# Performance work log

Hardware: AMD Instinct MI355X
Metric: run time of the kernel (lower is better)

The kernel has to match this reference:

```python
import jax, jax.numpy as jnp
import numpy as np

N = 100000   # nodes
E = 800000   # edges (avg degree 8)
D = 384      # feature dim (fixed by GraphConv(384,384))
OUT = 2      # out_channels


def setup_inputs() -> dict:
    key = jax.random.key(0)
    ks = jax.random.split(key, 10)
    s = 1.0 / np.sqrt(D)
    x = jax.random.normal(ks[0], (N, D), jnp.float32)
    edge_index = jax.random.randint(ks[1], (2, E), 0, N, dtype=jnp.int64)
    edge_weight = jax.random.uniform(ks[2], (E,), jnp.float32)
    return {
        "x": x,
        "edge_index": edge_index,
        "edge_weight": edge_weight,
        "W_rel1": jax.random.normal(ks[3], (D, D), jnp.float32) * s,
        "b_rel1": jnp.zeros((D,), jnp.float32),
        "W_root1": jax.random.normal(ks[4], (D, D), jnp.float32) * s,
        "W_rel2": jax.random.normal(ks[5], (D, D), jnp.float32) * s,
        "b_rel2": jnp.zeros((D,), jnp.float32),
        "W_root2": jax.random.normal(ks[6], (D, D), jnp.float32) * s,
        "W_lin": jax.random.normal(ks[7], (D, OUT), jnp.float32) * s,
        "b_lin": jnp.zeros((OUT,), jnp.float32),
    }


def _graph_conv(x, src, dst, ew, W_rel, b_rel, W_root):
    # PyG GraphConv (aggr='mean'): lin_rel(mean_j(ew_j * x_src_j)) + lin_root(x)
    msgs = ew[:, None] * x[src]                                   # [E, D] gather
    agg = jax.ops.segment_sum(msgs, dst, num_segments=N)          # [N, D] scatter
    cnt = jax.ops.segment_sum(jnp.ones_like(ew), dst, num_segments=N)
    mean = agg / jnp.maximum(cnt, 1.0)[:, None]
    return mean @ W_rel + b_rel + x @ W_root


def reference(x, edge_index, edge_weight,
              W_rel1, b_rel1, W_root1,
              W_rel2, b_rel2, W_root2,
              W_lin, b_lin):
    src, dst = edge_index[0], edge_index[1]
    h = jax.nn.relu(_graph_conv(x, src, dst, edge_weight, W_rel1, b_rel1, W_root1))
    # dropout(p=0.3) is identity in eval mode
    y = jax.nn.relu(_graph_conv(h, src, dst, edge_weight, W_rel2, b_rel2, W_root2))
    out = jax.nn.sigmoid(y @ W_lin + b_lin)                        # [N, OUT]
    return (out, y)
```

## Files before the change

### kernel.cpp

```cpp
#include <hip/hip_runtime.h>
#include <hip/hip_bf16.h>

typedef __bf16 bf16_t;
typedef bf16_t bf16x8 __attribute__((ext_vector_type(8)));
typedef float f32x4 __attribute__((ext_vector_type(4)));

typedef __attribute__((address_space(3))) unsigned int lds_u32;
typedef __attribute__((address_space(1))) unsigned int glb_u32;

__device__ __forceinline__ float bflo(unsigned int p){ union{unsigned int u; float f;} c; c.u = p << 16; return c.f; }
__device__ __forceinline__ float bfhi(unsigned int p){ union{unsigned int u; float f;} c; c.u = p & 0xffff0000u; return c.f; }
__device__ __forceinline__ unsigned int f2bfu(float f){
  union{float f; unsigned int u;} c; c.f = f;
  return (c.u + 0x7fffu + ((c.u >> 16) & 1u)) >> 16;
}

__global__ void k_cast_x(const float4* __restrict__ x, uint2* __restrict__ xb, int nq){
  int stride = gridDim.x * blockDim.x;
  for (int i = blockIdx.x * blockDim.x + threadIdx.x; i < nq; i += stride){
    float4 v = x[i];
    uint2 o;
    o.x = f2bfu(v.x) | (f2bfu(v.y) << 16);
    o.y = f2bfu(v.z) | (f2bfu(v.w) << 16);
    xb[i] = o;
  }
}

__global__ void k_castT_w4(const float* __restrict__ W0, const float* __restrict__ W1,
                           const float* __restrict__ W2, const float* __restrict__ W3,
                           unsigned short* __restrict__ T0, unsigned short* __restrict__ T1,
                           unsigned short* __restrict__ T2, unsigned short* __restrict__ T3){
  const float* W; unsigned short* T;
  switch (blockIdx.y){
    case 0: W = W0; T = T0; break;
    case 1: W = W1; T = T1; break;
    case 2: W = W2; T = T2; break;
    default: W = W3; T = T3; break;
  }
  int idx = blockIdx.x * 256 + threadIdx.x;
  int k = idx / 384, n = idx - k * 384;
  T[n * 384 + k] = (unsigned short)f2bfu(W[idx]);
}

__global__ void k_deg(const int* __restrict__ dst, int* __restrict__ deg, int E){
  int stride = gridDim.x * blockDim.x;
  for (int e = blockIdx.x * blockDim.x + threadIdx.x; e < E; e += stride)
    atomicAdd(&deg[dst[e]], 1);
}

__global__ void k_scan1(const int* __restrict__ deg, int* __restrict__ incl,
                        int* __restrict__ bsum, int n){
  __shared__ int wsum[16];
  int t = threadIdx.x, l = t & 63, w = t >> 6;
  int i = blockIdx.x * 1024 + t;
  int v = (i < n) ? deg[i] : 0;
  int xv = v;
  #pragma unroll
  for (int s = 1; s < 64; s <<= 1){
    int y = __shfl_up(xv, s, 64);
    if (l >= s) xv += y;
  }
  if (l == 63) wsum[w] = xv;
  __syncthreads();
  int off = 0;
  for (int k2 = 0; k2 < w; ++k2) off += wsum[k2];
  if (i < n) incl[i] = off + xv;
  if (t == 0){
    int tot = 0;
    for (int k2 = 0; k2 < 16; ++k2) tot += wsum[k2];
    bsum[blockIdx.x] = tot;
  }
}

__global__ void k_scan2(int* __restrict__ bsum, int nb){
  __shared__ int wtot;
  int t = threadIdx.x, l = t & 63, w = t >> 6;
  int v = (t < nb) ? bsum[t] : 0;
  int xv = v;
  #pragma unroll
  for (int s = 1; s < 64; s <<= 1){
    int y = __shfl_up(xv, s, 64);
    if (l >= s) xv += y;
  }
  if (t == 63) wtot = xv;
  __syncthreads();
  int off = (w == 1) ? wtot : 0;
  if (t < nb) bsum[t] = off + xv - v;
}

__global__ void k_scan3(const int* __restrict__ incl, const int* __restrict__ bsum,
                        const int* __restrict__ deg, int* __restrict__ rowptr,
                        int* __restrict__ cursor, int n){
  int i = blockIdx.x * 256 + threadIdx.x;
  if (i < n){
    int r = incl[i] + bsum[i >> 10];
    rowptr[i + 1] = r;
    cursor[i] = r - deg[i];
  }
  if (i == 0) rowptr[0] = 0;
}

__global__ void k_fill(const int* __restrict__ src, const int* __restrict__ dst, const float* __restrict__ ew,
                       int* __restrict__ cursor, int2* __restrict__ csr, int E){
  int stride = gridDim.x * blockDim.x;
  for (int e = blockIdx.x * blockDim.x + threadIdx.x; e < E; e += stride){
    int d = dst[e];
    int pos = atomicAdd(&cursor[d], 1);
    int2 c; c.x = src[e]; c.y = __float_as_int(ew[e]);
    csr[pos] = c;
  }
}

__global__ void k_agg(const unsigned short* __restrict__ X, unsigned short* __restrict__ OUT,
                      const int* __restrict__ rowptr, const int2* __restrict__ csr, int n_nodes){
  int w = threadIdx.x >> 6, l = threadIdx.x & 63;
  int node = blockIdx.x * 4 + w;
  if (node >= n_nodes) return;
  int e0 = rowptr[node], e1 = rowptr[node + 1];
  float a0=0,a1=0,a2=0,a3=0,a4=0,a5=0;
  const unsigned int* X32 = (const unsigned int*)X;
  int e = e0;
  for (; e + 2 <= e1; e += 2){
    int2 c0 = csr[e], c1 = csr[e + 1];
    const unsigned int* x0 = X32 + (long)c0.x * 192;
    const unsigned int* x1 = X32 + (long)c1.x * 192;
    unsigned int p0 = x0[l], p1 = x0[l + 64], p2 = x0[l + 128];
    unsigned int q0 = x1[l], q1 = x1[l + 64], q2 = x1[l + 128];
    float w0 = __int_as_float(c0.y), w1 = __int_as_float(c1.y);
    a0 += w0 * bflo(p0); a1 += w0 * bfhi(p0);
    a2 += w0 * bflo(p1); a3 += w0 * bfhi(p1);
    a4 += w0 * bflo(p2); a5 += w0 * bfhi(p2);
    a0 += w1 * bflo(q0); a1 += w1 * bfhi(q0);
    a2 += w1 * bflo(q1); a3 += w1 * bfhi(q1);
    a4 += w1 * bflo(q2); a5 += w1 * bfhi(q2);
  }
  if (e < e1){
    int2 c0 = csr[e];
    const unsigned int* x0 = X32 + (long)c0.x * 192;
    unsigned int p0 = x0[l], p1 = x0[l + 64], p2 = x0[l + 128];
    float w0 = __int_as_float(c0.y);
    a0 += w0 * bflo(p0); a1 += w0 * bfhi(p0);
    a2 += w0 * bflo(p1); a3 += w0 * bfhi(p1);
    a4 += w0 * bflo(p2); a5 += w0 * bfhi(p2);
  }
  int degn = e1 - e0;
  float inv = 1.0f / (float)(degn > 1 ? degn : 1);
  unsigned int* O32 = (unsigned int*)OUT + (long)node * 192;
  O32[l]       = f2bfu(a0 * inv) | (f2bfu(a1 * inv) << 16);
  O32[l + 64]  = f2bfu(a2 * inv) | (f2bfu(a3 * inv) << 16);
  O32[l + 128] = f2bfu(a4 * inv) | (f2bfu(a5 * inv) << 16);
}

template<int OUT_BF16>
__global__ __launch_bounds__(256) void k_gemm(
    const unsigned short* __restrict__ A1, const unsigned short* __restrict__ B1,
    const unsigned short* __restrict__ A2, const unsigned short* __restrict__ B2,
    const float* __restrict__ bias, void* __restrict__ Cout, int NN, int q, int r)
{
  __shared__ __align__(16) unsigned short lsA[2 * 128 * 32];
  __shared__ __align__(16) unsigned short lsB[2 * 128 * 32];
  int t = threadIdx.x;
  int w = t >> 6, l = t & 63;

  int lin = blockIdx.y * 3 + blockIdx.x;
  int xcd = lin & 7, idx = lin >> 3;
  int nl = idx + ((xcd < r) ? xcd * (q + 1) : r * (q + 1) + (xcd - r) * q);
  int mt = nl / 3, nt = nl - mt * 3;
  int m0 = mt * 128;
  int n0 = nt * 128;
  int wrow = (w & 1) * 64, wcol = (w >> 1) * 64;

  f32x4 acc[4][4] = {};

  int ar = t >> 2, ac = t & 3;
  int sw = (ar >> 1) & 3;
  int acs = (ac ^ sw) * 8;
  int ra0 = m0 + ar;       if (ra0 >= NN) ra0 = NN - 1;
  int ra1 = m0 + 64 + ar;  if (ra1 >= NN) ra1 = NN - 1;
  int rb0 = n0 + ar, rb1 = n0 + 64 + ar;

  char* lsAb = (char*)lsA;
  char* lsBb = (char*)lsB;

#define STAGE(buf, kk) do { \
    const unsigned short* Ag = ((kk) < 12) ? A1 : A2; \
    const unsigned short* Bg = ((kk) < 12) ? B1 : B2; \
    int kc = ((((kk) < 12) ? (kk) : (kk) - 12) << 5) + acs; \
    __builtin_amdgcn_global_load_lds((glb_u32*)(Ag + (long)ra0 * 384 + kc), (lds_u32*)(lsAb + (buf) * 8192 + w * 1024), 16, 0, 0); \
    __builtin_amdgcn_global_load_lds((glb_u32*)(Ag + (long)ra1 * 384 + kc), (lds_u32*)(lsAb + (buf) * 8192 + 4096 + w * 1024), 16, 0, 0); \
    __builtin_amdgcn_global_load_lds((glb_u32*)(Bg + (long)rb0 * 384 + kc), (lds_u32*)(lsBb + (buf) * 8192 + w * 1024), 16, 0, 0); \
    __builtin_amdgcn_global_load_lds((glb_u32*)(Bg + (long)rb1 * 384 + kc), (lds_u32*)(lsBb + (buf) * 8192 + 4096 + w * 1024), 16, 0, 0); \
  } while (0)

  STAGE(0, 0);
  __syncthreads();

  int rA = wrow + (l & 15);
  int rB = wcol + (l & 15);
  int swA = (rA >> 1) & 3, swB = (rB >> 1) & 3;
  int kchunk = l >> 4;
  int offA = ((kchunk ^ swA) * 8);
  int offB = ((kchunk ^ swB) * 8);

  for (int kk = 0; kk < 24; ++kk){
    int cur = kk & 1;
    if (kk < 23) STAGE(cur ^ 1, kk + 1);
    const unsigned short* bA = lsA + cur * 4096;
    const unsigned short* bB = lsB + cur * 4096;
    bf16x8 af[4], bfr[4];
    #pragma unroll
    for (int mi = 0; mi < 4; ++mi) af[mi]  = *(const bf16x8*)&bA[(rA + mi * 16) * 32 + offA];
    #pragma unroll
    for (int ni = 0; ni < 4; ++ni) bfr[ni] = *(const bf16x8*)&bB[(rB + ni * 16) * 32 + offB];
    #pragma unroll
    for (int mi = 0; mi < 4; ++mi)
      #pragma unroll
      for (int ni = 0; ni < 4; ++ni)
        acc[mi][ni] = __builtin_amdgcn_mfma_f32_16x16x32_bf16(af[mi], bfr[ni], acc[mi][ni], 0, 0, 0);
    __syncthreads();
  }
#undef STAGE

  int colb = l & 15, rowb = (l >> 4) * 4;
  #pragma unroll
  for (int mi = 0; mi < 4; ++mi){
    #pragma unroll
    for (int ni = 0; ni < 4; ++ni){
      f32x4 v = acc[mi][ni];
      int col = n0 + wcol + ni * 16 + colb;
      float bcol = bias[col];
      #pragma unroll
      for (int rr = 0; rr < 4; ++rr){
        int row = m0 + wrow + mi * 16 + rowb + rr;
        if (row < NN){
          float val = fmaxf(v[rr] + bcol, 0.0f);
          if (OUT_BF16) ((unsigned short*)Cout)[(long)row * 384 + col] = (unsigned short)f2bfu(val);
          else          ((float*)Cout)[(long)row * 384 + col] = val;
        }
      }
    }
  }
}

__global__ void k_out(const float* __restrict__ Y, const float* __restrict__ WL,
                      const float* __restrict__ bl, float* __restrict__ out, int n_nodes){
  int w = threadIdx.x >> 6, l = threadIdx.x & 63;
  int node = blockIdx.x * 4 + w;
  if (node >= n_nodes) return;
  const float* yr = Y + (long)node * 384;
  float s0 = 0.f, s1 = 0.f;
  #pragma unroll
  for (int j = 0; j < 6; ++j){
    int d = l + 64 * j;
    float v = yr[d];
    s0 += v * WL[2 * d];
    s1 += v * WL[2 * d + 1];
  }
  #pragma unroll
  for (int m = 32; m; m >>= 1){
    s0 += __shfl_xor(s0, m);
    s1 += __shfl_xor(s1, m);
  }
  if (l == 0){
    out[(long)node * 2]     = 1.f / (1.f + expf(-(s0 + bl[0])));
    out[(long)node * 2 + 1] = 1.f / (1.f + expf(-(s1 + bl[1])));
  }
}

extern "C" void kernel_launch(void* const* d_in, const int* in_sizes, int n_in,
                              void* d_out, int out_size, void* d_ws, size_t ws_size,
                              hipStream_t stream) {
  const float* x      = (const float*)d_in[0];
  const int*   ei     = (const int*)d_in[1];
  const float* ew     = (const float*)d_in[2];
  const float* Wrel1  = (const float*)d_in[3];
  const float* brel1  = (const float*)d_in[4];
  const float* Wroot1 = (const float*)d_in[5];
  const float* Wrel2  = (const float*)d_in[6];
  const float* brel2  = (const float*)d_in[7];
  const float* Wroot2 = (const float*)d_in[8];
  const float* Wlin   = (const float*)d_in[9];
  const float* blin   = (const float*)d_in[10];

  const int NN = in_sizes[0] / 384;
  const int E  = in_sizes[2];
  const int* src = ei;
  const int* dst = ei + E;

  char* p = (char*)d_ws;
  auto carve = [&](size_t bytes) -> void* {
    void* r = (void*)p;
    p += (bytes + 255) & ~(size_t)255;
    return r;
  };
  int*   deg     = (int*)carve((size_t)NN * 4);
  int*   rowptr  = (int*)carve((size_t)(NN + 1) * 4);
  int*   cursor  = (int*)carve((size_t)NN * 4);
  int*   incl    = (int*)carve((size_t)NN * 4);
  int*   bsum    = (int*)carve(1024);
  int2*  csr     = (int2*)carve((size_t)E * 8);
  unsigned short* xb  = (unsigned short*)carve((size_t)NN * 384 * 2);
  unsigned short* m1b = (unsigned short*)carve((size_t)NN * 384 * 2);
  unsigned short* hb  = (unsigned short*)carve((size_t)NN * 384 * 2);
  unsigned short* WT1 = (unsigned short*)carve(384 * 384 * 2);
  unsigned short* WT2 = (unsigned short*)carve(384 * 384 * 2);
  unsigned short* WT3 = (unsigned short*)carve(384 * 384 * 2);
  unsigned short* WT4 = (unsigned short*)carve(384 * 384 * 2);

  float* out = (float*)d_out;
  float* Y   = out + (size_t)NN * 2;

  int nScanB = (NN + 1023) / 1024;

  hipMemsetAsync(deg, 0, (size_t)NN * 4, stream);
  k_cast_x<<<2048, 256, 0, stream>>>((const float4*)x, (uint2*)xb, NN * 96);
  dim3 wg(576, 4);
  k_castT_w4<<<wg, 256, 0, stream>>>(Wrel1, Wroot1, Wrel2, Wroot2, WT1, WT2, WT3, WT4);
  k_deg<<<1024, 256, 0, stream>>>(dst, deg, E);
  k_scan1<<<nScanB, 1024, 0, stream>>>(deg, incl, bsum, NN);
  k_scan2<<<1, 128, 0, stream>>>(bsum, nScanB);
  k_scan3<<<(NN + 255) / 256, 256, 0, stream>>>(incl, bsum, deg, rowptr, cursor, NN);
  k_fill<<<1024, 256, 0, stream>>>(src, dst, ew, cursor, csr, E);

  int aggBlocks = (NN + 3) / 4;
  k_agg<<<aggBlocks, 256, 0, stream>>>(xb, m1b, rowptr, csr, NN);

  int gy = (NN + 127) / 128;
  int nwg = 3 * gy, q = nwg >> 3, r = nwg & 7;
  dim3 ggrid(3, gy);
  k_gemm<1><<<ggrid, 256, 0, stream>>>(m1b, WT1, xb, WT2, brel1, (void*)hb, NN, q, r);

  k_agg<<<aggBlocks, 256, 0, stream>>>(hb, m1b, rowptr, csr, NN);

  k_gemm<0><<<ggrid, 256, 0, stream>>>(m1b, WT3, hb, WT4, brel2, (void*)Y, NN, q, r);

  k_out<<<aggBlocks, 256, 0, stream>>>(Y, Wlin, blin, out, NN);
}
```

Baseline: 590.4 us.

## Restructure GEMM: direct B loads, K=64 steps, LDS-staged epilogue, fused output head

The GEMM now stages only the A tile in LDS with 64-wide K steps and an XOR swizzle. The B fragments are loaded straight from global memory into registers, and the K loop is fully unrolled with explicit waitcnt and barriers. The bf16 epilogue goes through LDS so stores are coalesced 16-byte writes. The second GEMM also computes the final linear projection, using shuffle reductions and atomicAdds into a logits buffer, and this replaces the separate k_out kernel that reread Y. In exchange it adds a memset and a small sigmoid kernel, plus atomic contention across the three column tiles.

```diff
diff --git a/kernel.cpp b/kernel.cpp
--- a/kernel.cpp
+++ b/kernel.cpp
@@ -155,116 +155,147 @@
 __global__ __launch_bounds__(256) void k_gemm(
     const unsigned short* __restrict__ A1, const unsigned short* __restrict__ B1,
     const unsigned short* __restrict__ A2, const unsigned short* __restrict__ B2,
-    const float* __restrict__ bias, void* __restrict__ Cout, int NN, int q, int r)
+    const float* __restrict__ bias, void* __restrict__ Cout,
+    const float* __restrict__ WL, float* __restrict__ olog,
+    int NN, int q, int r)
 {
-  __shared__ __align__(16) unsigned short lsA[2 * 128 * 32];
-  __shared__ __align__(16) unsigned short lsB[2 * 128 * 32];
+  __shared__ __align__(16) unsigned short lsA[2 * 128 * 64];
   int t = threadIdx.x;
   int w = t >> 6, l = t & 63;
 
-  int lin = blockIdx.y * 3 + blockIdx.x;
+  int lin = blockIdx.x;
   int xcd = lin & 7, idx = lin >> 3;
   int nl = idx + ((xcd < r) ? xcd * (q + 1) : r * (q + 1) + (xcd - r) * q);
   int mt = nl / 3, nt = nl - mt * 3;
-  int m0 = mt * 128;
-  int n0 = nt * 128;
+  int m0 = mt * 128, n0 = nt * 128;
   int wrow = (w & 1) * 64, wcol = (w >> 1) * 64;
 
   f32x4 acc[4][4] = {};
 
-  int ar = t >> 2, ac = t & 3;
-  int sw = (ar >> 1) & 3;
-  int acs = (ac ^ sw) * 8;
-  int ra0 = m0 + ar;       if (ra0 >= NN) ra0 = NN - 1;
-  int ra1 = m0 + 64 + ar;  if (ra1 >= NN) ra1 = NN - 1;
-  int rb0 = n0 + ar, rb1 = n0 + 64 + ar;
-
-  char* lsAb = (char*)lsA;
-  char* lsBb = (char*)lsB;
-
-#define STAGE(buf, kk) do { \
-    const unsigned short* Ag = ((kk) < 12) ? A1 : A2; \
-    const unsigned short* Bg = ((kk) < 12) ? B1 : B2; \
-    int kc = ((((kk) < 12) ? (kk) : (kk) - 12) << 5) + acs; \
-    __builtin_amdgcn_global_load_lds((glb_u32*)(Ag + (long)ra0 * 384 + kc), (lds_u32*)(lsAb + (buf) * 8192 + w * 1024), 16, 0, 0); \
-    __builtin_amdgcn_global_load_lds((glb_u32*)(Ag + (long)ra1 * 384 + kc), (lds_u32*)(lsAb + (buf) * 8192 + 4096 + w * 1024), 16, 0, 0); \
-    __builtin_amdgcn_global_load_lds((glb_u32*)(Bg + (long)rb0 * 384 + kc), (lds_u32*)(lsBb + (buf) * 8192 + w * 1024), 16, 0, 0); \
-    __builtin_amdgcn_global_load_lds((glb_u32*)(Bg + (long)rb1 * 384 + kc), (lds_u32*)(lsBb + (buf) * 8192 + 4096 + w * 1024), 16, 0, 0); \
+  int srow = t >> 3, sj = t & 7;
+  int sjx = sj ^ (srow & 7);
+
+  int rAb = wrow + (l & 15);
+  int jx  = (l & 15) & 7;
+  int kq  = l >> 4;
+  int rB  = n0 + wcol + (l & 15);
+  int koff = kq * 8;
+
+#define STAGE(buf, kk_) do { \
+    const unsigned short* Ag_ = ((kk_) < 6) ? A1 : A2; \
+    int kc_ = (((kk_) < 6) ? (kk_) : (kk_) - 6) << 6; \
+    _Pragma("unroll") \
+    for (int p_ = 0; p_ < 4; ++p_){ \
+      int ra_ = m0 + p_ * 32 + srow; if (ra_ >= NN) ra_ = NN - 1; \
+      __builtin_amdgcn_global_load_lds((glb_u32*)(Ag_ + (long)ra_ * 384 + kc_ + sjx * 8), \
+          (lds_u32*)((char*)lsA + (buf) * 16384 + p_ * 4096 + w * 1024), 16, 0, 0); \
+    } \
   } while (0)
 
   STAGE(0, 0);
-  __syncthreads();
-
-  int rA = wrow + (l & 15);
-  int rB = wcol + (l & 15);
-  int swA = (rA >> 1) & 3, swB = (rB >> 1) & 3;
-  int kchunk = l >> 4;
-  int offA = ((kchunk ^ swA) * 8);
-  int offB = ((kchunk ^ swB) * 8);
-
-  for (int kk = 0; kk < 24; ++kk){
+
+  #pragma unroll
+  for (int kk = 0; kk < 12; ++kk){
     int cur = kk & 1;
-    if (kk < 23) STAGE(cur ^ 1, kk + 1);
-    const unsigned short* bA = lsA + cur * 4096;
-    const unsigned short* bB = lsB + cur * 4096;
-    bf16x8 af[4], bfr[4];
-    #pragma unroll
-    for (int mi = 0; mi < 4; ++mi) af[mi]  = *(const bf16x8*)&bA[(rA + mi * 16) * 32 + offA];
-    #pragma unroll
-    for (int ni = 0; ni < 4; ++ni) bfr[ni] = *(const bf16x8*)&bB[(rB + ni * 16) * 32 + offB];
+    asm volatile("s_waitcnt vmcnt(0)" ::: "memory");
+    asm volatile("s_barrier" ::: "memory");
+    __builtin_amdgcn_sched_barrier(0);
+
+    const unsigned short* Bg = (kk < 6) ? B1 : B2;
+    int kc = ((kk < 6) ? kk : kk - 6) << 6;
+    bf16x8 bfr[2][4];
+    #pragma unroll
+    for (int s = 0; s < 2; ++s)
+      #pragma unroll
+      for (int ni = 0; ni < 4; ++ni)
+        bfr[s][ni] = *(const bf16x8*)&Bg[(long)(rB + ni * 16) * 384 + kc + s * 32 + koff];
+    __builtin_amdgcn_sched_barrier(0);
+
+    if (kk < 11) STAGE(cur ^ 1, kk + 1);
+    __builtin_amdgcn_sched_barrier(0);
+
+    const char* bA = (const char*)lsA + cur * 16384;
+    #pragma unroll
+    for (int s = 0; s < 2; ++s){
+      bf16x8 af[4];
+      #pragma unroll
+      for (int mi = 0; mi < 4; ++mi)
+        af[mi] = *(const bf16x8*)(bA + ((rAb + mi * 16) << 7) + ((((s << 2) + kq) ^ jx) << 4));
+      #pragma unroll
+      for (int mi = 0; mi < 4; ++mi)
+        #pragma unroll
+        for (int ni = 0; ni < 4; ++ni)
+          acc[mi][ni] = __builtin_amdgcn_mfma_f32_16x16x32_bf16(af[mi], bfr[s][ni], acc[mi][ni], 0, 0, 0);
+    }
+  }
+#undef STAGE
+
+  int colb = l & 15;
+  if (OUT_BF16){
+    __syncthreads();
+    unsigned short* lr = (unsigned short*)lsA;
     #pragma unroll
     for (int mi = 0; mi < 4; ++mi)
       #pragma unroll
-      for (int ni = 0; ni < 4; ++ni)
-        acc[mi][ni] = __builtin_amdgcn_mfma_f32_16x16x32_bf16(af[mi], bfr[ni], acc[mi][ni], 0, 0, 0);
-    __syncthreads();
-  }
-#undef STAGE
-
-  int colb = l & 15, rowb = (l >> 4) * 4;
-  #pragma unroll
-  for (int mi = 0; mi < 4; ++mi){
-    #pragma unroll
-    for (int ni = 0; ni < 4; ++ni){
-      f32x4 v = acc[mi][ni];
-      int col = n0 + wcol + ni * 16 + colb;
-      float bcol = bias[col];
-      #pragma unroll
-      for (int rr = 0; rr < 4; ++rr){
-        int row = m0 + wrow + mi * 16 + rowb + rr;
-        if (row < NN){
-          float val = fmaxf(v[rr] + bcol, 0.0f);
-          if (OUT_BF16) ((unsigned short*)Cout)[(long)row * 384 + col] = (unsigned short)f2bfu(val);
-          else          ((float*)Cout)[(long)row * 384 + col] = val;
+      for (int ni = 0; ni < 4; ++ni){
+        f32x4 v = acc[mi][ni];
+        int col = wcol + ni * 16 + colb;
+        float bcol = bias[n0 + col];
+        #pragma unroll
+        for (int rr = 0; rr < 4; ++rr){
+          int row = wrow + mi * 16 + kq * 4 + rr;
+          lr[row * 128 + col] = (unsigned short)f2bfu(fmaxf(v[rr] + bcol, 0.0f));
         }
       }
+    __syncthreads();
+    unsigned short* Cb = (unsigned short*)Cout;
+    #pragma unroll
+    for (int p = 0; p < 8; ++p){
+      int idx16 = p * 256 + t;
+      int row = idx16 >> 4, chunk = idx16 & 15;
+      int rg = m0 + row;
+      if (rg < NN)
+        *(uint4*)((char*)Cb + (long)rg * 768 + n0 * 2 + chunk * 16) =
+            *(const uint4*)((const char*)lsA + idx16 * 16);
     }
-  }
-}
-
-__global__ void k_out(const float* __restrict__ Y, const float* __restrict__ WL,
-                      const float* __restrict__ bl, float* __restrict__ out, int n_nodes){
-  int w = threadIdx.x >> 6, l = threadIdx.x & 63;
-  int node = blockIdx.x * 4 + w;
-  if (node >= n_nodes) return;
-  const float* yr = Y + (long)node * 384;
-  float s0 = 0.f, s1 = 0.f;
-  #pragma unroll
-  for (int j = 0; j < 6; ++j){
-    int d = l + 64 * j;
-    float v = yr[d];
-    s0 += v * WL[2 * d];
-    s1 += v * WL[2 * d + 1];
-  }
-  #pragma unroll
-  for (int m = 32; m; m >>= 1){
-    s0 += __shfl_xor(s0, m);
-    s1 += __shfl_xor(s1, m);
-  }
-  if (l == 0){
-    out[(long)node * 2]     = 1.f / (1.f + expf(-(s0 + bl[0])));
-    out[(long)node * 2 + 1] = 1.f / (1.f + expf(-(s1 + bl[1])));
-  }
+  } else {
+    float* Cf = (float*)Cout;
+    #pragma unroll
+    for (int mi = 0; mi < 4; ++mi){
+      float po[4][2] = {};
+      #pragma unroll
+      for (int ni = 0; ni < 4; ++ni){
+        f32x4 v = acc[mi][ni];
+        int col = n0 + wcol + ni * 16 + colb;
+        float bcol = bias[col];
+        float w0 = WL[col * 2], w1 = WL[col * 2 + 1];
+        #pragma unroll
+        for (int rr = 0; rr < 4; ++rr){
+          int row = m0 + wrow + mi * 16 + kq * 4 + rr;
+          float val = fmaxf(v[rr] + bcol, 0.0f);
+          if (row < NN) Cf[(long)row * 384 + col] = val;
+          po[rr][0] += val * w0;
+          po[rr][1] += val * w1;
+        }
+      }
+      #pragma unroll
+      for (int rr = 0; rr < 4; ++rr)
+        #pragma unroll
+        for (int o = 0; o < 2; ++o){
+          float v = po[rr][o];
+          v += __shfl_xor(v, 1); v += __shfl_xor(v, 2);
+          v += __shfl_xor(v, 4); v += __shfl_xor(v, 8);
+          int row = m0 + wrow + mi * 16 + kq * 4 + rr;
+          if (colb == 0 && row < NN) atomicAdd(&olog[row * 2 + o], v);
+        }
+    }
+  }
+}
+
+__global__ void k_sig(const float* __restrict__ olog, const float* __restrict__ bl,
+                      float* __restrict__ out, int n2){
+  int i = blockIdx.x * 256 + threadIdx.x;
+  if (i < n2) out[i] = 1.f / (1.f + expf(-(olog[i] + bl[i & 1])));
 }
 
 extern "C" void kernel_launch(void* const* d_in, const int* in_sizes, int n_in,
@@ -298,6 +329,7 @@
   int*   cursor  = (int*)carve((size_t)NN * 4);
   int*   incl    = (int*)carve((size_t)NN * 4);
   int*   bsum    = (int*)carve(1024);
+  float* olog    = (float*)carve((size_t)NN * 2 * 4);
   int2*  csr     = (int2*)carve((size_t)E * 8);
   unsigned short* xb  = (unsigned short*)carve((size_t)NN * 384 * 2);
   unsigned short* m1b = (unsigned short*)carve((size_t)NN * 384 * 2);
@@ -313,6 +345,7 @@
   int nScanB = (NN + 1023) / 1024;
 
   hipMemsetAsync(deg, 0, (size_t)NN * 4, stream);
+  hipMemsetAsync(olog, 0, (size_t)NN * 8, stream);
   k_cast_x<<<2048, 256, 0, stream>>>((const float4*)x, (uint2*)xb, NN * 96);
   dim3 wg(576, 4);
   k_castT_w4<<<wg, 256, 0, stream>>>(Wrel1, Wroot1, Wrel2, Wroot2, WT1, WT2, WT3, WT4);
@@ -325,14 +358,15 @@
   int aggBlocks = (NN + 3) / 4;
   k_agg<<<aggBlocks, 256, 0, stream>>>(xb, m1b, rowptr, csr, NN);
 
-  int gy = (NN + 127) / 128;
-  int nwg = 3 * gy, q = nwg >> 3, r = nwg & 7;
-  dim3 ggrid(3, gy);
-  k_gemm<1><<<ggrid, 256, 0, stream>>>(m1b, WT1, xb, WT2, brel1, (void*)hb, NN, q, r);
+  int nwg = 3 * ((NN + 127) / 128);
+  int q = nwg >> 3, r = nwg & 7;
+  k_gemm<1><<<nwg, 256, 0, stream>>>(m1b, WT1, xb, WT2, brel1, (void*)hb,
+                                     nullptr, nullptr, NN, q, r);
 
   k_agg<<<aggBlocks, 256, 0, stream>>>(hb, m1b, rowptr, csr, NN);
 
-  k_gemm<0><<<ggrid, 256, 0, stream>>>(m1b, WT3, hb, WT4, brel2, (void*)Y, NN, q, r);
-
-  k_out<<<aggBlocks, 256, 0, stream>>>(Y, Wlin, blin, out, NN);
-}
+  k_gemm<0><<<nwg, 256, 0, stream>>>(m1b, WT3, hb, WT4, brel2, (void*)Y,
+                                     Wlin, olog, NN, q, r);
+
+  k_sig<<<(NN * 2 + 255) / 256, 256, 0, stream>>>(olog, blin, out, NN * 2);
+}
```

Result: slower. 654.2 us (+10.8%).
